# Kernel tuning notes

Hardware: AMD Instinct MI355X
Metric: run time of the kernel (lower is better)

## Reference

```python
import jax, jax.numpy as jnp
import numpy as np

Q_HEADS, KV_HEADS, HEAD_SIZE, H, MAX_LEN = 16, 4, 64, 1024, 4096
B, S = 1, 4096


def _rope_tables(max_len, head_size):
    half = head_size // 2
    inv_freq = 1.0 / (10000.0 ** (np.arange(half, dtype=np.float32) / half))
    pos = np.arange(max_len, dtype=np.float32)
    ang = pos[:, None] * inv_freq[None, :]  # [max_len, half]
    return jnp.asarray(np.sin(ang)), jnp.asarray(np.cos(ang))


def setup_inputs() -> dict:
    key = jax.random.key(0)
    ks = jax.random.split(key, 6)
    sc = 1.0 / np.sqrt(H)
    x = jax.random.normal(ks[0], (B, S, H), dtype=jnp.float32)
    wq = jax.random.normal(ks[1], (H, H), dtype=jnp.float32) * sc
    wk = jax.random.normal(ks[2], (H, KV_HEADS * HEAD_SIZE), dtype=jnp.float32) * sc
    wv = jax.random.normal(ks[3], (H, KV_HEADS * HEAD_SIZE), dtype=jnp.float32) * sc
    wo = jax.random.normal(ks[4], (H, H), dtype=jnp.float32) * sc
    sin, cos = _rope_tables(MAX_LEN, HEAD_SIZE)
    full_mask = jnp.tril(jnp.ones((MAX_LEN, MAX_LEN), dtype=bool))
    attention_mask = jnp.ones((B, S), dtype=jnp.int32)
    return {"x": x, "attention_mask": attention_mask, "start": 0,
            "wq": wq, "wk": wk, "wv": wv, "wo": wo,
            "sin": sin, "cos": cos, "full_mask": full_mask}


def _rotate(t, sin, cos, start):
    # t: [b, heads, s, head_size]; interleaved even/odd RoPE
    s = t.shape[2]
    sn = sin[start:start + s, :][None, None, :, :]
    cs = cos[start:start + s, :][None, None, :, :]
    even, odd = t[..., 0::2], t[..., 1::2]
    out_even = cs * even - sn * odd
    out_odd = sn * even + cs * odd
    return jnp.stack((out_even, out_odd), axis=-1).reshape(t.shape)


def _expand_kv(t, group):
    # [b, kv_heads, s, d] -> [b, kv_heads*group, s, d]
    b, kvh, s, d = t.shape
    return jnp.broadcast_to(t[:, :, None], (b, kvh, group, s, d)).reshape(b, kvh * group, s, d)


def reference(x, attention_mask, start, wq, wk, wv, wo, sin, cos, full_mask):
    b, s, _ = x.shape
    group = Q_HEADS // KV_HEADS
    Q = (x @ wq).reshape(b, s, Q_HEADS, HEAD_SIZE).transpose(0, 2, 1, 3)
    K = (x @ wk).reshape(b, s, KV_HEADS, HEAD_SIZE).transpose(0, 2, 1, 3)
    V = (x @ wv).reshape(b, s, KV_HEADS, HEAD_SIZE).transpose(0, 2, 1, 3)
    Q = _rotate(Q, sin, cos, start)
    K = _rotate(K, sin, cos, start)
    K = _expand_kv(K, group)
    V = _expand_kv(V, group)
    z = jnp.einsum('bhqd,bhkd->bhqk', Q, K) / (HEAD_SIZE ** 0.5)
    kv_len = start + s
    mask = full_mask[:s, :kv_len][None, None, :, :]
    amask = (attention_mask[:, :kv_len] != 0)[:, None, None, :]
    mask = mask & amask
    z = jnp.where(mask, z, -1000000.0)
    A = jax.nn.softmax(z, axis=-1)
    ctx = jnp.einsum('bhqk,bhkd->bhqd', A, V)
    q_mask = attention_mask[:, :s].astype(ctx.dtype)[:, None, :, None]
    ctx = ctx * q_mask
    ctx = ctx.transpose(0, 2, 1, 3).reshape(b, s, H)
    return ctx @ wo
```

## Files before the change

kernel.cpp:

```cpp
#include <hip/hip_runtime.h>

typedef __bf16 bf16x8 __attribute__((ext_vector_type(8)));
typedef float f32x4 __attribute__((ext_vector_type(4)));
typedef unsigned int u32x4 __attribute__((ext_vector_type(4)));

typedef const void __attribute__((address_space(1)))* gas1;
typedef void __attribute__((address_space(3)))* las3;

__device__ __forceinline__ unsigned short f2bf(float f) {
  unsigned int u = __builtin_bit_cast(unsigned int, f);
  u += 0x7fffu + ((u >> 16) & 1u);
  return (unsigned short)(u >> 16);
}
__device__ __forceinline__ float bf2f(unsigned short h) {
  unsigned int u = ((unsigned int)h) << 16;
  return __builtin_bit_cast(float, u);
}
__device__ __forceinline__ unsigned int pack2bf(float lo, float hi) {
  return (unsigned int)f2bf(lo) | ((unsigned int)f2bf(hi) << 16);
}
__device__ __forceinline__ unsigned int packtr(float lo, float hi) {
  return __builtin_amdgcn_perm(__builtin_bit_cast(unsigned int, hi),
                               __builtin_bit_cast(unsigned int, lo), 0x07060302u);
}

__global__ __launch_bounds__(256) void prep(const float* __restrict__ x,
                                            const float* __restrict__ wq,
                                            const float* __restrict__ wk,
                                            const float* __restrict__ wv,
                                            const float* __restrict__ wo,
                                            const float* __restrict__ sinT,
                                            const float* __restrict__ cosT,
                                            unsigned short* __restrict__ xb,
                                            unsigned short* __restrict__ wtqkv,
                                            unsigned short* __restrict__ wot,
                                            float2* __restrict__ scT) {
  __shared__ float tile[32][33];
  const int b = blockIdx.x;
  const int tid = threadIdx.x;
  if (b < 4096) {
    int i = b * 256 + tid;
    float4 v = ((const float4*)x)[i];
    uint2 o;
    o.x = pack2bf(v.x, v.y);
    o.y = pack2bf(v.z, v.w);
    ((uint2*)xb)[i] = o;
    return;
  }
  if (b >= 6656) {
    int idx = (b - 6656) * 256 + tid;
    scT[idx] = make_float2(sinT[idx], cosT[idx]);
    return;
  }
  const float* src;
  unsigned short* dst;
  int R, C, t;
  if (b < 5120)      { t = b - 4096; src = wq; dst = wtqkv;               R = 1024; C = 1024; }
  else if (b < 5376) { t = b - 5120; src = wk; dst = wtqkv + 1024 * 1024; R = 1024; C = 256; }
  else if (b < 5632) { t = b - 5376; src = wv; dst = wtqkv + 1280 * 1024; R = 1024; C = 256; }
  else               { t = b - 5632; src = wo; dst = wot;                 R = 1024; C = 1024; }
  const int ntc = C >> 5;
  const int c0 = (t % ntc) * 32, r0 = (t / ntc) * 32;
  const int tx = tid & 31, ty = tid >> 5;
#pragma unroll
  for (int i = 0; i < 4; ++i)
    tile[ty + i * 8][tx] = src[(r0 + ty + i * 8) * C + c0 + tx];
  __syncthreads();
#pragma unroll
  for (int i = 0; i < 4; ++i)
    dst[(c0 + ty + i * 8) * R + r0 + tx] = f2bf(tile[tx][ty + i * 8]);
}

__global__ __launch_bounds__(256, 3) void gemm_qkv(const unsigned short* __restrict__ A,
                                                   const unsigned short* __restrict__ Bt,
                                                   const float2* __restrict__ scT,
                                                   unsigned short* __restrict__ Qh,
                                                   unsigned short* __restrict__ Kh,
                                                   unsigned short* __restrict__ Vt) {
  __shared__ __align__(16) unsigned short Als[128 * 32];
  __shared__ __align__(16) unsigned short Bls[64 * 32];
  const int K = 1024;
  const int tid = threadIdx.x;
  const int wave = tid >> 6, lane = tid & 63;
  const int lgrp = lane >> 4, lmod = lane & 15;
  const int wm = (wave & 1) * 64, wn = (wave >> 1) * 32;
  const int m0 = blockIdx.y * 128, n0 = blockIdx.x * 64;
  const int rr = tid >> 2, cc = (tid & 3) * 8;

  f32x4 acc[4][2] = {};

  for (int k0 = 0; k0 < K; k0 += 32) {
    __syncthreads();
#pragma unroll
    for (int it = 0; it < 2; ++it) {
      int idx = tid + it * 256;
      __builtin_amdgcn_global_load_lds((gas1)(const void*)&A[(size_t)(m0 + (idx >> 2)) * K + k0 + cc],
                                       (las3)(void*)&Als[(it * 256 + wave * 64) * 8], 16, 0, 0);
    }
    __builtin_amdgcn_global_load_lds((gas1)(const void*)&Bt[(size_t)(n0 + rr) * K + k0 + cc],
                                     (las3)(void*)&Bls[(wave * 64) * 8], 16, 0, 0);
    __syncthreads();
    bf16x8 af[4], bfr[2];
#pragma unroll
    for (int mi = 0; mi < 4; ++mi)
      af[mi] = __builtin_bit_cast(bf16x8, *(const u32x4*)&Als[(wm + mi * 16 + lmod) * 32 + lgrp * 8]);
#pragma unroll
    for (int ni = 0; ni < 2; ++ni)
      bfr[ni] = __builtin_bit_cast(bf16x8, *(const u32x4*)&Bls[(wn + ni * 16 + lmod) * 32 + lgrp * 8]);
#pragma unroll
    for (int mi = 0; mi < 4; ++mi)
#pragma unroll
      for (int ni = 0; ni < 2; ++ni)
        acc[mi][ni] = __builtin_amdgcn_mfma_f32_16x16x32_bf16(af[mi], bfr[ni], acc[mi][ni], 0, 0, 0);
  }

  const int cbase = n0;
  if (cbase >= 1280) {
    const int kvh = (cbase - 1280) >> 6;
#pragma unroll
    for (int mi = 0; mi < 4; ++mi)
#pragma unroll
      for (int ni = 0; ni < 2; ++ni) {
        int d = wn + ni * 16 + lmod;
        int s = m0 + wm + mi * 16 + lgrp * 4;
        uint2 o;
        o.x = pack2bf(acc[mi][ni][0], acc[mi][ni][1]);
        o.y = pack2bf(acc[mi][ni][2], acc[mi][ni][3]);
        *(uint2*)&Vt[((size_t)(kvh * 64 + d)) * 4096 + s] = o;
      }
    return;
  }

  const float qscale = 0.18033688011112042f;
  const bool isQ = (cbase < 1024);
  const int h = isQ ? (cbase >> 6) : ((cbase - 1024) >> 6);
  unsigned short* dstbase = isQ ? Qh : Kh;
  const bool evn = (lmod & 1) == 0;
#pragma unroll
  for (int mi = 0; mi < 4; ++mi)
#pragma unroll
    for (int ni = 0; ni < 2; ++ni) {
      int d = ((cbase & 63) + wn + ni * 16 + lmod) & 63;
      int i = d >> 1;
#pragma unroll
      for (int r = 0; r < 4; ++r) {
        float v = acc[mi][ni][r];
        float pp = __shfl_xor(v, 1, 64);
        int rl = wm + mi * 16 + lgrp * 4 + r;
        float2 sc = scT[(size_t)(m0 + rl) * 32 + i];
        float e = evn ? v : pp, o = evn ? pp : v;
        float outv = evn ? (sc.y * e - sc.x * o) : (sc.x * e + sc.y * o);
        if (isQ) outv *= qscale;
        dstbase[((size_t)h * 4096 + m0 + rl) * 64 + d] = f2bf(outv);
      }
    }
}

__global__ __launch_bounds__(256, 3) void gemm_out(const unsigned short* __restrict__ A,
                                                   const unsigned short* __restrict__ Bt,
                                                   float* __restrict__ Cout) {
  __shared__ __align__(16) unsigned short Als[128 * 32];
  __shared__ __align__(16) unsigned short Bls[64 * 32];
  const int K = 1024, N = 1024;
  const int tid = threadIdx.x;
  const int wave = tid >> 6, lane = tid & 63;
  const int lgrp = lane >> 4, lmod = lane & 15;
  const int wm = (wave & 1) * 64, wn = (wave >> 1) * 32;
  const int m0 = blockIdx.y * 128, n0 = blockIdx.x * 64;
  const int rr = tid >> 2, cc = (tid & 3) * 8;

  f32x4 acc[4][2] = {};

  for (int k0 = 0; k0 < K; k0 += 32) {
    __syncthreads();
#pragma unroll
    for (int it = 0; it < 2; ++it) {
      int idx = tid + it * 256;
      __builtin_amdgcn_global_load_lds((gas1)(const void*)&A[(size_t)(m0 + (idx >> 2)) * K + k0 + cc],
                                       (las3)(void*)&Als[(it * 256 + wave * 64) * 8], 16, 0, 0);
    }
    __builtin_amdgcn_global_load_lds((gas1)(const void*)&Bt[(size_t)(n0 + rr) * K + k0 + cc],
                                     (las3)(void*)&Bls[(wave * 64) * 8], 16, 0, 0);
    __syncthreads();
    bf16x8 af[4], bfr[2];
#pragma unroll
    for (int mi = 0; mi < 4; ++mi)
      af[mi] = __builtin_bit_cast(bf16x8, *(const u32x4*)&Als[(wm + mi * 16 + lmod) * 32 + lgrp * 8]);
#pragma unroll
    for (int ni = 0; ni < 2; ++ni)
      bfr[ni] = __builtin_bit_cast(bf16x8, *(const u32x4*)&Bls[(wn + ni * 16 + lmod) * 32 + lgrp * 8]);
#pragma unroll
    for (int mi = 0; mi < 4; ++mi)
#pragma unroll
      for (int ni = 0; ni < 2; ++ni)
        acc[mi][ni] = __builtin_amdgcn_mfma_f32_16x16x32_bf16(af[mi], bfr[ni], acc[mi][ni], 0, 0, 0);
  }

#pragma unroll
  for (int mi = 0; mi < 4; ++mi)
#pragma unroll
    for (int ni = 0; ni < 2; ++ni)
#pragma unroll
      for (int r = 0; r < 4; ++r) {
        int row = m0 + wm + mi * 16 + lgrp * 4 + r;
        int col = n0 + wn + ni * 16 + lmod;
        Cout[(size_t)row * N + col] = acc[mi][ni][r];
      }
}

__global__ __launch_bounds__(128, 4) void attn7(const unsigned short* __restrict__ Qh,
                                                const unsigned short* __restrict__ Kh,
                                                const unsigned short* __restrict__ Vt,
                                                unsigned short* __restrict__ ctx) {
  __shared__ __align__(16) unsigned short Kls[128 * 68];
  __shared__ __align__(16) unsigned short Vls[64 * 136];
  const int bx = blockIdx.x;
  const int head = bx & 15;
  const int qidx = bx >> 4;
  int qb64;
  if (qidx < 16)      qb64 = 63 - qidx;
  else if (qidx < 32) qb64 = 16 + qidx - 16 + 16;
  else if (qidx < 48) qb64 = 63 - qidx;
  else                qb64 = qidx - 48;
  const int kvh = head >> 2;
  const int tid = threadIdx.x;
  const int wave = tid >> 6, lane = tid & 63;
  const int lgrp = lane >> 4, lmod = lane & 15;
  const int qbase = qb64 * 64;
  const int nch = (qb64 >> 1) + 1;

  const unsigned short* Kg = Kh + (size_t)kvh * 4096 * 64;
  const unsigned short* Vg = Vt + (size_t)kvh * 64 * 4096;

  bf16x8 qf[2][2];
  int qrow[2];
#pragma unroll
  for (int qt = 0; qt < 2; ++qt) {
    qrow[qt] = qbase + wave * 32 + qt * 16 + lmod;
    const unsigned short* Qg = Qh + ((size_t)head * 4096 + qrow[qt]) * 64;
    qf[qt][0] = __builtin_bit_cast(bf16x8, *(const u32x4*)&Qg[lgrp * 8]);
    qf[qt][1] = __builtin_bit_cast(bf16x8, *(const u32x4*)&Qg[32 + lgrp * 8]);
  }

  const int kbase = (8 * (lmod >> 2) + (lmod & 3)) * 68 + lgrp * 8;
  const int vbase = lmod * 136 + lgrp * 8;

  f32x4 accO[2][4] = {};
  float m_i[2] = {-3e38f, -3e38f}, l_i[2] = {0.f, 0.f};

  for (int kc = 0; kc < nch; ++kc) {
    const int kb = kc * 128;
    __syncthreads();
#pragma unroll
    for (int i = 0; i < 8; ++i) {
      int ii = tid + i * 128;
      int r = ii >> 3, sg = (ii & 7) * 8;
      u32x4 dK = *(const u32x4*)&Kg[(size_t)(kb + r) * 64 + sg];
      uint2* pd = (uint2*)&Kls[r * 68 + sg];
      pd[0] = make_uint2(dK[0], dK[1]);
      pd[1] = make_uint2(dK[2], dK[3]);
    }
#pragma unroll
    for (int i = 0; i < 8; ++i) {
      int ii = tid + i * 128;
      int r = ii >> 4, sg = (ii & 15) * 8;
      *(u32x4*)&Vls[r * 136 + sg] = *(const u32x4*)&Vg[(size_t)r * 4096 + kb + sg];
    }
    __syncthreads();

    f32x4 s[4][2][2];
#pragma unroll
    for (int g = 0; g < 4; ++g)
#pragma unroll
      for (int t = 0; t < 2; ++t) {
        const unsigned short* ka = &Kls[kbase + (32 * g + 4 * t) * 68];
        uint2 a0 = *(const uint2*)&ka[0];
        uint2 a1 = *(const uint2*)&ka[4];
        uint2 b0 = *(const uint2*)&ka[32];
        uint2 b1 = *(const uint2*)&ka[36];
        u32x4 lo = {a0.x, a0.y, a1.x, a1.y};
        u32x4 hi = {b0.x, b0.y, b1.x, b1.y};
        bf16x8 alo = __builtin_bit_cast(bf16x8, lo);
        bf16x8 ahi = __builtin_bit_cast(bf16x8, hi);
#pragma unroll
        for (int qt = 0; qt < 2; ++qt) {
          f32x4 z = {};
          z = __builtin_amdgcn_mfma_f32_16x16x32_bf16(alo, qf[qt][0], z, 0, 0, 0);
          z = __builtin_amdgcn_mfma_f32_16x16x32_bf16(ahi, qf[qt][1], z, 0, 0, 0);
          s[g][t][qt] = z;
        }
      }

#pragma unroll
    for (int qt = 0; qt < 2; ++qt) {
      if (kb + 127 > qbase + wave * 32 + qt * 16) {
#pragma unroll
        for (int g = 0; g < 4; ++g)
#pragma unroll
          for (int t = 0; t < 2; ++t)
#pragma unroll
            for (int r = 0; r < 4; ++r) {
              int key = kb + 32 * g + 8 * lgrp + 4 * t + r;
              if (key > qrow[qt]) s[g][t][qt][r] = -3e38f;
            }
      }
    }

#pragma unroll
    for (int qt = 0; qt < 2; ++qt) {
      f32x4 v0 = s[0][0][qt], v1 = s[0][1][qt];
#pragma unroll
      for (int g = 1; g < 4; ++g)
#pragma unroll
        for (int r = 0; r < 4; ++r) {
          v0[r] = fmaxf(v0[r], s[g][0][qt][r]);
          v1[r] = fmaxf(v1[r], s[g][1][qt][r]);
        }
      float mx = fmaxf(fmaxf(fmaxf(v0[0], v0[1]), fmaxf(v0[2], v0[3])),
                       fmaxf(fmaxf(v1[0], v1[1]), fmaxf(v1[2], v1[3])));
      mx = fmaxf(mx, __shfl_xor(mx, 16, 64));
      mx = fmaxf(mx, __shfl_xor(mx, 32, 64));
      float mnew = fmaxf(m_i[qt], mx);
      float alpha = __builtin_amdgcn_exp2f(m_i[qt] - mnew);
      m_i[qt] = mnew;
      f32x4 su = {};
#pragma unroll
      for (int g = 0; g < 4; ++g)
#pragma unroll
        for (int t = 0; t < 2; ++t)
#pragma unroll
          for (int r = 0; r < 4; ++r) {
            float ev = __builtin_amdgcn_exp2f(s[g][t][qt][r] - mnew);
            s[g][t][qt][r] = ev;
            su[r] += ev;
          }
      float rs = (su[0] + su[1]) + (su[2] + su[3]);
      rs += __shfl_xor(rs, 16, 64);
      rs += __shfl_xor(rs, 32, 64);
      l_i[qt] = l_i[qt] * alpha + rs;
#pragma unroll
      for (int dt = 0; dt < 4; ++dt)
#pragma unroll
        for (int r = 0; r < 4; ++r) accO[qt][dt][r] *= alpha;
    }

#pragma unroll
    for (int g = 0; g < 4; ++g) {
      bf16x8 pf[2];
#pragma unroll
      for (int qt = 0; qt < 2; ++qt) {
        u32x4 pk;
        pk[0] = packtr(s[g][0][qt][0], s[g][0][qt][1]);
        pk[1] = packtr(s[g][0][qt][2], s[g][0][qt][3]);
        pk[2] = packtr(s[g][1][qt][0], s[g][1][qt][1]);
        pk[3] = packtr(s[g][1][qt][2], s[g][1][qt][3]);
        pf[qt] = __builtin_bit_cast(bf16x8, pk);
      }
#pragma unroll
      for (int dt = 0; dt < 4; ++dt) {
        bf16x8 vf = __builtin_bit_cast(bf16x8, *(const u32x4*)&Vls[vbase + dt * 2176 + 32 * g]);
        accO[0][dt] = __builtin_amdgcn_mfma_f32_16x16x32_bf16(vf, pf[0], accO[0][dt], 0, 0, 0);
        accO[1][dt] = __builtin_amdgcn_mfma_f32_16x16x32_bf16(vf, pf[1], accO[1][dt], 0, 0, 0);
      }
    }
  }

#pragma unroll
  for (int qt = 0; qt < 2; ++qt) {
    float inv = 1.f / l_i[qt];
#pragma unroll
    for (int dt = 0; dt < 4; ++dt) {
      uint2 o;
      o.x = pack2bf(accO[qt][dt][0] * inv, accO[qt][dt][1] * inv);
      o.y = pack2bf(accO[qt][dt][2] * inv, accO[qt][dt][3] * inv);
      *(uint2*)&ctx[(size_t)qrow[qt] * 1024 + head * 64 + dt * 16 + lgrp * 4] = o;
    }
  }
}

extern "C" void kernel_launch(void* const* d_in, const int* in_sizes, int n_in,
                              void* d_out, int out_size, void* d_ws, size_t ws_size,
                              hipStream_t stream) {
  const float* x    = (const float*)d_in[0];
  const float* wq   = (const float*)d_in[3];
  const float* wk   = (const float*)d_in[4];
  const float* wv   = (const float*)d_in[5];
  const float* wo   = (const float*)d_in[6];
  const float* sinT = (const float*)d_in[7];
  const float* cosT = (const float*)d_in[8];

  unsigned short* ws    = (unsigned short*)d_ws;
  unsigned short* xb    = ws;
  unsigned short* wtqkv = xb + 4096 * 1024;
  unsigned short* wot   = wtqkv + 1536 * 1024;
  unsigned short* Qh    = wot + 1024 * 1024;
  unsigned short* Kh    = Qh + 16 * 4096 * 64;
  unsigned short* Vt    = Kh + 4 * 4096 * 64;
  unsigned short* ctx   = Vt + 4 * 64 * 4096;
  float2* scT           = (float2*)(ctx + 4096 * 1024);
  float* out = (float*)d_out;

  prep<<<7168, 256, 0, stream>>>(x, wq, wk, wv, wo, sinT, cosT, xb, wtqkv, wot, scT);
  gemm_qkv<<<dim3(24, 32), 256, 0, stream>>>(xb, wtqkv, scT, Qh, Kh, Vt);
  attn7<<<dim3(1024), 128, 0, stream>>>(Qh, Kh, Vt, ctx);
  gemm_out<<<dim3(16, 32), 256, 0, stream>>>(ctx, wot, out);
}
```

Baseline: 269.1 us.

## Switch GEMMs to single-wave 64x64 tiles and attention to 256-thread 128-row blocks

Both GEMM kernels move from 256-thread blocks on 128x64 tiles to one wave per block on 64x64 tiles, with each wave holding a 4x4 MFMA accumulator. This doubles the grid and gives each wave more reuse of its fragments, but drops the sharing of LDS tiles across waves. The attention kernel goes from 128-thread blocks on 64 query rows to 256-thread blocks on 128 query rows, with a simpler causal block ordering. That halves the number of attention blocks and the K/V reloads per query row, at some cost to load balance and occupancy.

```diff
diff --git a/kernel.cpp b/kernel.cpp
--- a/kernel.cpp
+++ b/kernel.cpp
@@ -71,58 +71,54 @@
     dst[(c0 + ty + i * 8) * R + r0 + tx] = f2bf(tile[tx][ty + i * 8]);
 }
 
-__global__ __launch_bounds__(256, 3) void gemm_qkv(const unsigned short* __restrict__ A,
-                                                   const unsigned short* __restrict__ Bt,
-                                                   const float2* __restrict__ scT,
-                                                   unsigned short* __restrict__ Qh,
-                                                   unsigned short* __restrict__ Kh,
-                                                   unsigned short* __restrict__ Vt) {
-  __shared__ __align__(16) unsigned short Als[128 * 32];
+__global__ __launch_bounds__(64, 4) void gemm_qkv(const unsigned short* __restrict__ A,
+                                                  const unsigned short* __restrict__ Bt,
+                                                  const float2* __restrict__ scT,
+                                                  unsigned short* __restrict__ Qh,
+                                                  unsigned short* __restrict__ Kh,
+                                                  unsigned short* __restrict__ Vt) {
+  __shared__ __align__(16) unsigned short Als[64 * 32];
   __shared__ __align__(16) unsigned short Bls[64 * 32];
   const int K = 1024;
-  const int tid = threadIdx.x;
-  const int wave = tid >> 6, lane = tid & 63;
+  const int lane = threadIdx.x;
   const int lgrp = lane >> 4, lmod = lane & 15;
-  const int wm = (wave & 1) * 64, wn = (wave >> 1) * 32;
-  const int m0 = blockIdx.y * 128, n0 = blockIdx.x * 64;
-  const int rr = tid >> 2, cc = (tid & 3) * 8;
-
-  f32x4 acc[4][2] = {};
+  const int m0 = blockIdx.y * 64, n0 = blockIdx.x * 64;
+  const int lr = lane >> 2, lc = (lane & 3) * 8;
+
+  f32x4 acc[4][4] = {};
 
   for (int k0 = 0; k0 < K; k0 += 32) {
     __syncthreads();
 #pragma unroll
-    for (int it = 0; it < 2; ++it) {
-      int idx = tid + it * 256;
-      __builtin_amdgcn_global_load_lds((gas1)(const void*)&A[(size_t)(m0 + (idx >> 2)) * K + k0 + cc],
-                                       (las3)(void*)&Als[(it * 256 + wave * 64) * 8], 16, 0, 0);
-    }
-    __builtin_amdgcn_global_load_lds((gas1)(const void*)&Bt[(size_t)(n0 + rr) * K + k0 + cc],
-                                     (las3)(void*)&Bls[(wave * 64) * 8], 16, 0, 0);
-    __syncthreads();
-    bf16x8 af[4], bfr[2];
-#pragma unroll
-    for (int mi = 0; mi < 4; ++mi)
-      af[mi] = __builtin_bit_cast(bf16x8, *(const u32x4*)&Als[(wm + mi * 16 + lmod) * 32 + lgrp * 8]);
-#pragma unroll
-    for (int ni = 0; ni < 2; ++ni)
-      bfr[ni] = __builtin_bit_cast(bf16x8, *(const u32x4*)&Bls[(wn + ni * 16 + lmod) * 32 + lgrp * 8]);
-#pragma unroll
-    for (int mi = 0; mi < 4; ++mi)
-#pragma unroll
-      for (int ni = 0; ni < 2; ++ni)
+    for (int i = 0; i < 4; ++i) {
+      __builtin_amdgcn_global_load_lds((gas1)(const void*)&A[(size_t)(m0 + i * 16 + lr) * K + k0 + lc],
+                                       (las3)(void*)&Als[i * 512], 16, 0, 0);
+      __builtin_amdgcn_global_load_lds((gas1)(const void*)&Bt[(size_t)(n0 + i * 16 + lr) * K + k0 + lc],
+                                       (las3)(void*)&Bls[i * 512], 16, 0, 0);
+    }
+    __syncthreads();
+    bf16x8 af[4], bfr[4];
+#pragma unroll
+    for (int mi = 0; mi < 4; ++mi)
+      af[mi] = __builtin_bit_cast(bf16x8, *(const u32x4*)&Als[(mi * 16 + lmod) * 32 + lgrp * 8]);
+#pragma unroll
+    for (int ni = 0; ni < 4; ++ni)
+      bfr[ni] = __builtin_bit_cast(bf16x8, *(const u32x4*)&Bls[(ni * 16 + lmod) * 32 + lgrp * 8]);
+#pragma unroll
+    for (int mi = 0; mi < 4; ++mi)
+#pragma unroll
+      for (int ni = 0; ni < 4; ++ni)
         acc[mi][ni] = __builtin_amdgcn_mfma_f32_16x16x32_bf16(af[mi], bfr[ni], acc[mi][ni], 0, 0, 0);
   }
 
-  const int cbase = n0;
-  if (cbase >= 1280) {
-    const int kvh = (cbase - 1280) >> 6;
-#pragma unroll
-    for (int mi = 0; mi < 4; ++mi)
-#pragma unroll
-      for (int ni = 0; ni < 2; ++ni) {
-        int d = wn + ni * 16 + lmod;
-        int s = m0 + wm + mi * 16 + lgrp * 4;
+  if (n0 >= 1280) {
+    const int kvh = (n0 - 1280) >> 6;
+#pragma unroll
+    for (int mi = 0; mi < 4; ++mi)
+#pragma unroll
+      for (int ni = 0; ni < 4; ++ni) {
+        int d = ni * 16 + lmod;
+        int s = m0 + mi * 16 + lgrp * 4;
         uint2 o;
         o.x = pack2bf(acc[mi][ni][0], acc[mi][ni][1]);
         o.y = pack2bf(acc[mi][ni][2], acc[mi][ni][3]);
@@ -132,21 +128,21 @@
   }
 
   const float qscale = 0.18033688011112042f;
-  const bool isQ = (cbase < 1024);
-  const int h = isQ ? (cbase >> 6) : ((cbase - 1024) >> 6);
+  const bool isQ = (n0 < 1024);
+  const int h = isQ ? (n0 >> 6) : ((n0 - 1024) >> 6);
   unsigned short* dstbase = isQ ? Qh : Kh;
   const bool evn = (lmod & 1) == 0;
 #pragma unroll
   for (int mi = 0; mi < 4; ++mi)
 #pragma unroll
-    for (int ni = 0; ni < 2; ++ni) {
-      int d = ((cbase & 63) + wn + ni * 16 + lmod) & 63;
+    for (int ni = 0; ni < 4; ++ni) {
+      int d = ni * 16 + lmod;
       int i = d >> 1;
 #pragma unroll
       for (int r = 0; r < 4; ++r) {
         float v = acc[mi][ni][r];
         float pp = __shfl_xor(v, 1, 64);
-        int rl = wm + mi * 16 + lgrp * 4 + r;
+        int rl = mi * 16 + lgrp * 4 + r;
         float2 sc = scT[(size_t)(m0 + rl) * 32 + i];
         float e = evn ? v : pp, o = evn ? pp : v;
         float outv = evn ? (sc.y * e - sc.x * o) : (sc.x * e + sc.y * o);
@@ -156,59 +152,56 @@
     }
 }
 
-__global__ __launch_bounds__(256, 3) void gemm_out(const unsigned short* __restrict__ A,
-                                                   const unsigned short* __restrict__ Bt,
-                                                   float* __restrict__ Cout) {
-  __shared__ __align__(16) unsigned short Als[128 * 32];
+__global__ __launch_bounds__(64, 4) void gemm_out(const unsigned short* __restrict__ A,
+                                                  const unsigned short* __restrict__ Bt,
+                                                  float* __restrict__ Cout) {
+  __shared__ __align__(16) unsigned short Als[64 * 32];
   __shared__ __align__(16) unsigned short Bls[64 * 32];
   const int K = 1024, N = 1024;
-  const int tid = threadIdx.x;
-  const int wave = tid >> 6, lane = tid & 63;
+  const int lane = threadIdx.x;
   const int lgrp = lane >> 4, lmod = lane & 15;
-  const int wm = (wave & 1) * 64, wn = (wave >> 1) * 32;
-  const int m0 = blockIdx.y * 128, n0 = blockIdx.x * 64;
-  const int rr = tid >> 2, cc = (tid & 3) * 8;
-
-  f32x4 acc[4][2] = {};
+  const int m0 = blockIdx.y * 64, n0 = blockIdx.x * 64;
+  const int lr = lane >> 2, lc = (lane & 3) * 8;
+
+  f32x4 acc[4][4] = {};
 
   for (int k0 = 0; k0 < K; k0 += 32) {
     __syncthreads();
 #pragma unroll
-    for (int it = 0; it < 2; ++it) {
-      int idx = tid + it * 256;
-      __builtin_amdgcn_global_load_lds((gas1)(const void*)&A[(size_t)(m0 + (idx >> 2)) * K + k0 + cc],
-                                       (las3)(void*)&Als[(it * 256 + wave * 64) * 8], 16, 0, 0);
-    }
-    __builtin_amdgcn_global_load_lds((gas1)(const void*)&Bt[(size_t)(n0 + rr) * K + k0 + cc],
-                                     (las3)(void*)&Bls[(wave * 64) * 8], 16, 0, 0);
-    __syncthreads();
-    bf16x8 af[4], bfr[2];
-#pragma unroll
-    for (int mi = 0; mi < 4; ++mi)
-      af[mi] = __builtin_bit_cast(bf16x8, *(const u32x4*)&Als[(wm + mi * 16 + lmod) * 32 + lgrp * 8]);
-#pragma unroll
-    for (int ni = 0; ni < 2; ++ni)
-      bfr[ni] = __builtin_bit_cast(bf16x8, *(const u32x4*)&Bls[(wn + ni * 16 + lmod) * 32 + lgrp * 8]);
-#pragma unroll
-    for (int mi = 0; mi < 4; ++mi)
-#pragma unroll
-      for (int ni = 0; ni < 2; ++ni)
+    for (int i = 0; i < 4; ++i) {
+      __builtin_amdgcn_global_load_lds((gas1)(const void*)&A[(size_t)(m0 + i * 16 + lr) * K + k0 + lc],
+                                       (las3)(void*)&Als[i * 512], 16, 0, 0);
+      __builtin_amdgcn_global_load_lds((gas1)(const void*)&Bt[(size_t)(n0 + i * 16 + lr) * K + k0 + lc],
+                                       (las3)(void*)&Bls[i * 512], 16, 0, 0);
+    }
+    __syncthreads();
+    bf16x8 af[4], bfr[4];
+#pragma unroll
+    for (int mi = 0; mi < 4; ++mi)
+      af[mi] = __builtin_bit_cast(bf16x8, *(const u32x4*)&Als[(mi * 16 + lmod) * 32 + lgrp * 8]);
+#pragma unroll
+    for (int ni = 0; ni < 4; ++ni)
+      bfr[ni] = __builtin_bit_cast(bf16x8, *(const u32x4*)&Bls[(ni * 16 + lmod) * 32 + lgrp * 8]);
+#pragma unroll
+    for (int mi = 0; mi < 4; ++mi)
+#pragma unroll
+      for (int ni = 0; ni < 4; ++ni)
         acc[mi][ni] = __builtin_amdgcn_mfma_f32_16x16x32_bf16(af[mi], bfr[ni], acc[mi][ni], 0, 0, 0);
   }
 
 #pragma unroll
   for (int mi = 0; mi < 4; ++mi)
 #pragma unroll
-    for (int ni = 0; ni < 2; ++ni)
+    for (int ni = 0; ni < 4; ++ni)
 #pragma unroll
       for (int r = 0; r < 4; ++r) {
-        int row = m0 + wm + mi * 16 + lgrp * 4 + r;
-        int col = n0 + wn + ni * 16 + lmod;
+        int row = m0 + mi * 16 + lgrp * 4 + r;
+        int col = n0 + ni * 16 + lmod;
         Cout[(size_t)row * N + col] = acc[mi][ni][r];
       }
 }
 
-__global__ __launch_bounds__(128, 4) void attn7(const unsigned short* __restrict__ Qh,
+__global__ __launch_bounds__(256, 2) void attn3(const unsigned short* __restrict__ Qh,
                                                 const unsigned short* __restrict__ Kh,
                                                 const unsigned short* __restrict__ Vt,
                                                 unsigned short* __restrict__ ctx) {
@@ -217,17 +210,12 @@
   const int bx = blockIdx.x;
   const int head = bx & 15;
   const int qidx = bx >> 4;
-  int qb64;
-  if (qidx < 16)      qb64 = 63 - qidx;
-  else if (qidx < 32) qb64 = 16 + qidx - 16 + 16;
-  else if (qidx < 48) qb64 = 63 - qidx;
-  else                qb64 = qidx - 48;
+  const int qb = (qidx < 16) ? (31 - qidx) : (qidx - 16);
   const int kvh = head >> 2;
   const int tid = threadIdx.x;
   const int wave = tid >> 6, lane = tid & 63;
   const int lgrp = lane >> 4, lmod = lane & 15;
-  const int qbase = qb64 * 64;
-  const int nch = (qb64 >> 1) + 1;
+  const int qbase = qb * 128;
 
   const unsigned short* Kg = Kh + (size_t)kvh * 4096 * 64;
   const unsigned short* Vg = Vt + (size_t)kvh * 64 * 4096;
@@ -248,12 +236,12 @@
   f32x4 accO[2][4] = {};
   float m_i[2] = {-3e38f, -3e38f}, l_i[2] = {0.f, 0.f};
 
-  for (int kc = 0; kc < nch; ++kc) {
+  for (int kc = 0; kc <= qb; ++kc) {
     const int kb = kc * 128;
     __syncthreads();
 #pragma unroll
-    for (int i = 0; i < 8; ++i) {
-      int ii = tid + i * 128;
+    for (int i = 0; i < 4; ++i) {
+      int ii = tid + i * 256;
       int r = ii >> 3, sg = (ii & 7) * 8;
       u32x4 dK = *(const u32x4*)&Kg[(size_t)(kb + r) * 64 + sg];
       uint2* pd = (uint2*)&Kls[r * 68 + sg];
@@ -261,8 +249,8 @@
       pd[1] = make_uint2(dK[2], dK[3]);
     }
 #pragma unroll
-    for (int i = 0; i < 8; ++i) {
-      int ii = tid + i * 128;
+    for (int i = 0; i < 4; ++i) {
+      int ii = tid + i * 256;
       int r = ii >> 4, sg = (ii & 15) * 8;
       *(u32x4*)&Vls[r * 136 + sg] = *(const u32x4*)&Vg[(size_t)r * 4096 + kb + sg];
     }
@@ -401,7 +389,7 @@
   float* out = (float*)d_out;
 
   prep<<<7168, 256, 0, stream>>>(x, wq, wk, wv, wo, sinT, cosT, xb, wtqkv, wot, scT);
-  gemm_qkv<<<dim3(24, 32), 256, 0, stream>>>(xb, wtqkv, scT, Qh, Kh, Vt);
-  attn7<<<dim3(1024), 128, 0, stream>>>(Qh, Kh, Vt, ctx);
-  gemm_out<<<dim3(16, 32), 256, 0, stream>>>(ctx, wot, out);
-}
+  gemm_qkv<<<dim3(24, 64), 64, 0, stream>>>(xb, wtqkv, scT, Qh, Kh, Vt);
+  attn3<<<dim3(512), 256, 0, stream>>>(Qh, Kh, Vt, ctx);
+  gemm_out<<<dim3(16, 64), 64, 0, stream>>>(ctx, wot, out);
+}
```

After: 249.7 us. 7.2% less time.
